# Performance work log

Hardware: AMD Instinct MI355X
Metric: run time of the kernel (lower is better)

## Reference

```python
import jax, jax.numpy as jnp
import numpy as np

B, S, NE, E, H = 4, 2048, 8, 1024, 16
DH = E // H


def setup_inputs() -> dict:
    key = jax.random.key(0)
    ks = jax.random.split(key, 10)
    s = 0.02
    return {
        "x": jax.random.normal(ks[0], (B, S, E), dtype=jnp.float32),
        "w1": jax.random.normal(ks[1], (NE, 4 * E, E), dtype=jnp.float32) * s,
        "b1": jnp.zeros((NE, 4 * E), dtype=jnp.float32),
        "w2": jax.random.normal(ks[2], (NE, E, 4 * E), dtype=jnp.float32) * s,
        "b2": jnp.zeros((NE, E), dtype=jnp.float32),
        "in_proj_w": jax.random.normal(ks[3], (3 * E, E), dtype=jnp.float32) * s,
        "in_proj_b": jnp.zeros((3 * E,), dtype=jnp.float32),
        "out_w": jax.random.normal(ks[4], (E, E), dtype=jnp.float32) * s,
        "out_b": jnp.zeros((E,), dtype=jnp.float32),
        "expert_id": 3,
    }


def reference(x, w1, b1, w2, b2, in_proj_w, in_proj_b, out_w, out_b, expert_id):
    # Per-expert FFN: [B,S,E] -> [B,S,NE,E]
    h = jax.nn.relu(jnp.einsum("bse,nfe->bsnf", x, w1) + b1)
    eo = jnp.einsum("bsnf,nef->bsne", h, w2) + b2  # [B,S,NE,E]

    # Multihead self-attention over the expert axis, batched over (B,S).
    wq, wk, wv = in_proj_w[:E], in_proj_w[E:2 * E], in_proj_w[2 * E:]
    bq, bk, bv = in_proj_b[:E], in_proj_b[E:2 * E], in_proj_b[2 * E:]
    q = (eo @ wq.T + bq).reshape(B, S, NE, H, DH)
    k = (eo @ wk.T + bk).reshape(B, S, NE, H, DH)
    v = (eo @ wv.T + bv).reshape(B, S, NE, H, DH)

    scale = 1.0 / jnp.sqrt(jnp.asarray(DH, dtype=q.dtype))
    # torch additive float mask: tril of ONES added to logits (not -inf masking)
    add_mask = jnp.tril(jnp.ones((NE, NE), dtype=q.dtype))
    logits = jnp.einsum("bsqhd,bskhd->bshqk", q, k) * scale + add_mask
    attn = jax.nn.softmax(logits, axis=-1)
    o = jnp.einsum("bshqk,bskhd->bsqhd", attn, v).reshape(B, S, NE, E)
    o = o @ out_w.T + out_b  # [B,S,NE,E]

    return o[:, :, expert_id, :]  # [B,S,E]
```

## Files before the change

### kernel.cpp

```cpp
#include <hip/hip_runtime.h>

typedef __bf16 bf16x8 __attribute__((ext_vector_type(8)));
typedef float  f32x4  __attribute__((ext_vector_type(4)));

__device__ __forceinline__ float bf2f(unsigned short u) {
    union { unsigned int i; float f; } x; x.i = ((unsigned int)u) << 16; return x.f;
}
__device__ __forceinline__ unsigned short f2bf(float f) {
    union { float f; unsigned int i; } x; x.f = f;
    unsigned int r = x.i + 0x7fff + ((x.i >> 16) & 1);
    return (unsigned short)(r >> 16);
}

__device__ __forceinline__ void gload16(const void* g, void* l) {
    __builtin_amdgcn_global_load_lds(
        (const __attribute__((address_space(1))) void*)g,
        (__attribute__((address_space(3))) void*)l, 16, 0, 0);
}

__global__ __launch_bounds__(256) void cvt_f32_bf16(
    const float4* __restrict__ in, ushort4* __restrict__ out, long n4)
{
    long i = (long)blockIdx.x * blockDim.x + threadIdx.x;
    const long stride = (long)gridDim.x * blockDim.x;
    for (; i < n4; i += stride) {
        const float4 v = in[i];
        ushort4 o = { f2bf(v.x), f2bf(v.y), f2bf(v.z), f2bf(v.w) };
        out[i] = o;
    }
}


template<bool RELU, typename CT>
__global__ __launch_bounds__(256, 4) void gemm_nt(
    const ushort* __restrict__ A, long lda, long sAz,
    const ushort* __restrict__ B, long ldb, long sBz,
    const float* __restrict__ bias, long sBiasz,
    CT* __restrict__ C, long ldc, long sCz,
    int K)
{
    const long z = blockIdx.z;
    A    += z * sAz;
    B    += z * sBz;
    bias += z * sBiasz;
    C    += z * sCz;

    __shared__ alignas(16) ushort As[128 * 32];
    __shared__ alignas(16) ushort Bs[128 * 32];

    const int t    = threadIdx.x;
    const int w    = t >> 6;
    const int lane = t & 63;
    const int lr   = lane & 15;
    const int lq   = lane >> 4;
    const int wm   = (w >> 1) * 64;
    const int wn   = (w & 1) * 64;
    const long m0  = (long)blockIdx.y * 128;
    const long n0  = (long)blockIdx.x * 128;

    const int srow   = t >> 2;
    const int schunk = (t & 3) * 8;
    const ushort* aG = A + (m0 + srow) * lda + schunk;
    const ushort* bG = B + (n0 + srow) * ldb + schunk;
    char* lA = (char*)As + w * 1024;
    char* lB = (char*)Bs + w * 1024;

    f32x4 acc[4][4];
#pragma unroll
    for (int i = 0; i < 4; i++)
#pragma unroll
        for (int j = 0; j < 4; j++) acc[i][j] = (f32x4){0.f, 0.f, 0.f, 0.f};

    for (int kt = 0; kt < K; kt += 32) {
        gload16(aG,            lA);
        gload16(aG + 64 * lda, lA + 4096);
        gload16(bG,            lB);
        gload16(bG + 64 * ldb, lB + 4096);
        aG += 32; bG += 32;
        __syncthreads();

        bf16x8 af[4], bf[4];
#pragma unroll
        for (int i = 0; i < 4; i++)
            af[i] = *(const bf16x8*)&As[(wm + i * 16 + lr) * 32 + lq * 8];
#pragma unroll
        for (int j = 0; j < 4; j++)
            bf[j] = *(const bf16x8*)&Bs[(wn + j * 16 + lr) * 32 + lq * 8];
#pragma unroll
        for (int i = 0; i < 4; i++)
#pragma unroll
            for (int j = 0; j < 4; j++)
                acc[i][j] = __builtin_amdgcn_mfma_f32_16x16x32_bf16(af[i], bf[j], acc[i][j], 0, 0, 0);
        __syncthreads();
    }

#pragma unroll
    for (int j = 0; j < 4; j++) {
        const long col = n0 + wn + j * 16 + lr;
        const float bv = bias[col];
#pragma unroll
        for (int i = 0; i < 4; i++) {
            const long rbase = m0 + wm + i * 16 + lq * 4;
#pragma unroll
            for (int r = 0; r < 4; r++) {
                float v = acc[i][j][r] + bv;
                if (RELU) v = fmaxf(v, 0.f);
                if constexpr (__is_same(CT, ushort)) C[(rbase + r) * ldc + col] = f2bf(v);
                else                                 C[(rbase + r) * ldc + col] = v;
            }
        }
    }
}

__global__ __launch_bounds__(256, 4) void gemm_qkv(
    const ushort* __restrict__ A, long lda, long sAz,
    const ushort* __restrict__ B, long ldb,
    const float* __restrict__ bias,
    ushort* __restrict__ qc,
    ushort* __restrict__ kvc,
    int K, const int* __restrict__ eid_p)
{
    const long z   = blockIdx.z;
    const long n0  = (long)blockIdx.x * 128;
    const bool isq = (n0 < 1024);
    if (isq && z != (long)(*eid_p)) return;
    A += z * sAz;

    __shared__ alignas(16) ushort As[128 * 32];
    __shared__ alignas(16) ushort Bs[128 * 32];

    const int t    = threadIdx.x;
    const int w    = t >> 6;
    const int lane = t & 63;
    const int lr   = lane & 15;
    const int lq   = lane >> 4;
    const int wm   = (w >> 1) * 64;
    const int wn   = (w & 1) * 64;
    const long m0  = (long)blockIdx.y * 128;

    const int srow   = t >> 2;
    const int schunk = (t & 3) * 8;
    const ushort* aG = A + (m0 + srow) * lda + schunk;
    const ushort* bG = B + (n0 + srow) * ldb + schunk;
    char* lA = (char*)As + w * 1024;
    char* lB = (char*)Bs + w * 1024;

    f32x4 acc[4][4];
#pragma unroll
    for (int i = 0; i < 4; i++)
#pragma unroll
        for (int j = 0; j < 4; j++) acc[i][j] = (f32x4){0.f, 0.f, 0.f, 0.f};

    for (int kt = 0; kt < K; kt += 32) {
        gload16(aG,            lA);
        gload16(aG + 64 * lda, lA + 4096);
        gload16(bG,            lB);
        gload16(bG + 64 * ldb, lB + 4096);
        aG += 32; bG += 32;
        __syncthreads();

        bf16x8 af[4], bf[4];
#pragma unroll
        for (int i = 0; i < 4; i++)
            af[i] = *(const bf16x8*)&As[(wm + i * 16 + lr) * 32 + lq * 8];
#pragma unroll
        for (int j = 0; j < 4; j++)
            bf[j] = *(const bf16x8*)&Bs[(wn + j * 16 + lr) * 32 + lq * 8];
#pragma unroll
        for (int i = 0; i < 4; i++)
#pragma unroll
            for (int j = 0; j < 4; j++)
                acc[i][j] = __builtin_amdgcn_mfma_f32_16x16x32_bf16(af[i], bf[j], acc[i][j], 0, 0, 0);
        __syncthreads();
    }

#pragma unroll
    for (int j = 0; j < 4; j++) {
        const long col = n0 + wn + j * 16 + lr;
        const float bv = bias[col];
#pragma unroll
        for (int i = 0; i < 4; i++) {
            const long rbase = m0 + wm + i * 16 + lq * 4;
#pragma unroll
            for (int r = 0; r < 4; r++) {
                const float v = acc[i][j][r] + bv;
                const long row = rbase + r;
                if (isq) qc[row * 1024 + col] = f2bf(v);
                else     kvc[row * 16384 + z * 2048 + (col - 1024)] = f2bf(v);
            }
        }
    }
}

__global__ __launch_bounds__(256) void attn_kernel(
    const ushort* __restrict__ qc, const ushort* __restrict__ kvc,
    const int* __restrict__ eid_p, ushort* __restrict__ o3)
{
    const size_t m = blockIdx.x;
    const int t    = threadIdx.x;
    const int h    = t >> 4;
    const int d0   = (t & 15) * 4;
    const int eid  = *eid_p;

    const ushort4 qu = *(const ushort4*)(qc + m * 1024 + h * 64 + d0);
    const float qv[4] = { bf2f(qu.x), bf2f(qu.y), bf2f(qu.z), bf2f(qu.w) };

    float l[8];
#pragma unroll
    for (int n = 0; n < 8; n++) {
        const ushort4 ku = *(const ushort4*)(kvc + (m * 8 + n) * 2048 + h * 64 + d0);
        float p = qv[0] * bf2f(ku.x) + qv[1] * bf2f(ku.y) + qv[2] * bf2f(ku.z) + qv[3] * bf2f(ku.w);
        p += __shfl_xor(p, 1);
        p += __shfl_xor(p, 2);
        p += __shfl_xor(p, 4);
        p += __shfl_xor(p, 8);
        l[n] = p * 0.125f + ((n <= eid) ? 1.0f : 0.0f);
    }
    float mx = l[0];
#pragma unroll
    for (int n = 1; n < 8; n++) mx = fmaxf(mx, l[n]);
    float e[8], s = 0.f;
#pragma unroll
    for (int n = 0; n < 8; n++) { e[n] = __expf(l[n] - mx); s += e[n]; }
    const float inv = 1.f / s;

    float o[4] = {0.f, 0.f, 0.f, 0.f};
#pragma unroll
    for (int n = 0; n < 8; n++) {
        const ushort4 vu = *(const ushort4*)(kvc + (m * 8 + n) * 2048 + 1024 + h * 64 + d0);
        const float a = e[n] * inv;
        o[0] += a * bf2f(vu.x); o[1] += a * bf2f(vu.y);
        o[2] += a * bf2f(vu.z); o[3] += a * bf2f(vu.w);
    }
    ushort4 ou = { f2bf(o[0]), f2bf(o[1]), f2bf(o[2]), f2bf(o[3]) };
    *(ushort4*)(o3 + m * 1024 + h * 64 + d0) = ou;
}

extern "C" void kernel_launch(void* const* d_in, const int* in_sizes, int n_in,
                              void* d_out, int out_size, void* d_ws, size_t ws_size,
                              hipStream_t stream)
{
    const float* x   = (const float*)d_in[0];
    const float* w1  = (const float*)d_in[1];
    const float* b1  = (const float*)d_in[2];
    const float* w2  = (const float*)d_in[3];
    const float* b2  = (const float*)d_in[4];
    const float* ipw = (const float*)d_in[5];
    const float* ipb = (const float*)d_in[6];
    const float* ow  = (const float*)d_in[7];
    const float* ob  = (const float*)d_in[8];
    const int*   eid = (const int*)d_in[9];

    char* ws = (char*)d_ws;
    size_t off = 0;
    auto alloc = [&](size_t bytes) { char* p = ws + off; off += (bytes + 255) & ~(size_t)255; return p; };
    ushort* w1b  = (ushort*)alloc(8LL * 4096 * 1024 * 2);
    ushort* w2b  = (ushort*)alloc(8LL * 1024 * 4096 * 2);
    ushort* ipwb = (ushort*)alloc(3LL * 1024 * 1024 * 2);
    ushort* owb  = (ushort*)alloc(1LL * 1024 * 1024 * 2);
    ushort* xb   = (ushort*)alloc(8192LL * 1024 * 2);
    ushort* o3b  = (ushort*)alloc(8192LL * 1024 * 2);
    const size_t fixed = off;

    long Mc = 2048;
    while (Mc > 256 && fixed + (size_t)Mc * 116736 + 2048 > ws_size) Mc >>= 1;
    ushort* hb  = (ushort*)alloc((size_t)Mc * 8 * 4096 * 2);
    ushort* eob = (ushort*)alloc((size_t)Mc * 8 * 1024 * 2);
    ushort* kvc = (ushort*)alloc((size_t)Mc * 8 * 2048 * 2);
    ushort* qc  = (ushort*)alloc((size_t)Mc * 1024 * 2);

    const dim3 blk(256);
    const dim3 cgrid(2048);

    cvt_f32_bf16<<<cgrid, blk, 0, stream>>>((const float4*)w1,  (ushort4*)w1b,  8LL * 4096 * 1024 / 4);
    cvt_f32_bf16<<<cgrid, blk, 0, stream>>>((const float4*)w2,  (ushort4*)w2b,  8LL * 1024 * 4096 / 4);
    cvt_f32_bf16<<<cgrid, blk, 0, stream>>>((const float4*)ipw, (ushort4*)ipwb, 3LL * 1024 * 1024 / 4);
    cvt_f32_bf16<<<cgrid, blk, 0, stream>>>((const float4*)ow,  (ushort4*)owb,  1LL * 1024 * 1024 / 4);
    cvt_f32_bf16<<<cgrid, blk, 0, stream>>>((const float4*)x,   (ushort4*)xb,   8192LL * 1024 / 4);

    for (long m0 = 0; m0 < 8192; m0 += Mc) {
        const unsigned my = (unsigned)(Mc / 128);
        gemm_nt<true, ushort><<<dim3(32, my, 8), blk, 0, stream>>>(
            xb + m0 * 1024, 1024, 0,
            w1b, 1024, 4096LL * 1024,
            b1, 4096,
            hb, 4096, (long)Mc * 4096,
            1024);
        gemm_nt<false, ushort><<<dim3(8, my, 8), blk, 0, stream>>>(
            hb, 4096, (long)Mc * 4096,
            w2b, 4096, 1024LL * 4096,
            b2, 1024,
            eob, 1024, (long)Mc * 1024,
            4096);
        gemm_qkv<<<dim3(24, my, 8), blk, 0, stream>>>(
            eob, 1024, (long)Mc * 1024,
            ipwb, 1024,
            ipb,
            qc, kvc,
            1024, eid);
        attn_kernel<<<dim3((unsigned)Mc), blk, 0, stream>>>(
            qc, kvc, eid, o3b + m0 * 1024);
    }

    gemm_nt<false, float><<<dim3(8, 64, 1), blk, 0, stream>>>(
        o3b, 1024, 0,
        owb, 1024, 0,
        ob, 0,
        (float*)d_out, 1024, 0,
        1024);
}
```

Measured before the change: 2.406 ms.

## Replace 128x128 GEMMs with 256x256 4-stage pipelined swizzled-LDS GEMM kernel

Merges the generic GEMM and the QKV GEMM into one templated 256x256-tile kernel with 512 threads. It keeps a 4-deep ring of LDS buffers filled by async global-to-LDS loads, waiting on vmcnt counts instead of two full barriers per k-step. It also adds an XOR swizzle on the LDS layout to avoid bank conflicts, a workgroup-index remap across XCDs, and raised MFMA issue priority. The larger tiles raise arithmetic intensity but cut the number of workgroups and use more LDS and registers, which may lower occupancy.

```diff
diff --git a/kernel.cpp b/kernel.cpp
--- a/kernel.cpp
+++ b/kernel.cpp
@@ -30,163 +30,123 @@
     }
 }
 
-
-template<bool RELU, typename CT>
-__global__ __launch_bounds__(256, 4) void gemm_nt(
+template<bool RELU, typename CT, bool QKV>
+__global__ __launch_bounds__(512, 2) void gemm256(
     const ushort* __restrict__ A, long lda, long sAz,
     const ushort* __restrict__ B, long ldb, long sBz,
     const float* __restrict__ bias, long sBiasz,
     CT* __restrict__ C, long ldc, long sCz,
-    int K)
-{
-    const long z = blockIdx.z;
+    ushort* __restrict__ qc, ushort* __restrict__ kvc,
+    int K, const int* __restrict__ eid_p)
+{
+    const long z  = blockIdx.z;
+    const int gx  = gridDim.x;
+    const int nwg = gx * gridDim.y;
+    int wg = blockIdx.y * gx + blockIdx.x;
+    if ((nwg & 7) == 0) wg = (wg & 7) * (nwg >> 3) + (wg >> 3);
+    const long n0 = (long)(wg % gx) * 256;
+    const long m0 = (long)(wg / gx) * 256;
+
+    if constexpr (QKV) {
+        if (n0 < 1024 && z != (long)(*eid_p)) return;
+    }
     A    += z * sAz;
     B    += z * sBz;
     bias += z * sBiasz;
-    C    += z * sCz;
-
-    __shared__ alignas(16) ushort As[128 * 32];
-    __shared__ alignas(16) ushort Bs[128 * 32];
+    if constexpr (!QKV) C += z * sCz;
+
+    __shared__ alignas(16) ushort As[4][256 * 32];
+    __shared__ alignas(16) ushort Bs[4][256 * 32];
 
     const int t    = threadIdx.x;
-    const int w    = t >> 6;
+    const int wid  = t >> 6;
     const int lane = t & 63;
     const int lr   = lane & 15;
     const int lq   = lane >> 4;
-    const int wm   = (w >> 1) * 64;
-    const int wn   = (w & 1) * 64;
-    const long m0  = (long)blockIdx.y * 128;
-    const long n0  = (long)blockIdx.x * 128;
-
-    const int srow   = t >> 2;
-    const int schunk = (t & 3) * 8;
-    const ushort* aG = A + (m0 + srow) * lda + schunk;
-    const ushort* bG = B + (n0 + srow) * ldb + schunk;
-    char* lA = (char*)As + w * 1024;
-    char* lB = (char*)Bs + w * 1024;
-
-    f32x4 acc[4][4];
-#pragma unroll
-    for (int i = 0; i < 4; i++)
+    const int wr   = wid >> 2;
+    const int wc   = wid & 3;
+
+    const int d0 = wid * 1024 + lane * 16;
+    const int s0 = d0 ^ (((d0 >> 7) & 3) << 4);
+    const int r0 = s0 >> 6;
+    const int c0 = (s0 & 63) >> 1;
+    const ushort* aG0 = A + (m0 + r0) * lda + c0;
+    const ushort* aG1 = A + (m0 + r0 + 128) * lda + c0;
+    const ushort* bG0 = B + (n0 + r0) * ldb + c0;
+    const ushort* bG1 = B + (n0 + r0 + 128) * ldb + c0;
+    const int ldsOff = wid * 512;
+
+    const int chnk  = lq ^ ((lr >> 1) & 3);
+    const int aBase = (wr * 128 + lr) * 32 + chnk * 8;
+    const int bBase = (wc * 64  + lr) * 32 + chnk * 8;
+
+    const int nt = K >> 5;
+
+    #define STAGE(buf_, kt_) { \
+        const long ko_ = (long)(kt_) * 32; \
+        gload16(aG0 + ko_, (void*)&As[buf_][ldsOff]); \
+        gload16(aG1 + ko_, (void*)&As[buf_][4096 + ldsOff]); \
+        gload16(bG0 + ko_, (void*)&Bs[buf_][ldsOff]); \
+        gload16(bG1 + ko_, (void*)&Bs[buf_][4096 + ldsOff]); }
+
+    STAGE(0, 0)
+    if (nt > 1) STAGE(1, 1)
+    if (nt > 2) STAGE(2, 2)
+
+    f32x4 acc[8][4];
+#pragma unroll
+    for (int i = 0; i < 8; i++)
 #pragma unroll
         for (int j = 0; j < 4; j++) acc[i][j] = (f32x4){0.f, 0.f, 0.f, 0.f};
 
-    for (int kt = 0; kt < K; kt += 32) {
-        gload16(aG,            lA);
-        gload16(aG + 64 * lda, lA + 4096);
-        gload16(bG,            lB);
-        gload16(bG + 64 * ldb, lB + 4096);
-        aG += 32; bG += 32;
-        __syncthreads();
-
-        bf16x8 af[4], bf[4];
-#pragma unroll
-        for (int i = 0; i < 4; i++)
-            af[i] = *(const bf16x8*)&As[(wm + i * 16 + lr) * 32 + lq * 8];
-#pragma unroll
-        for (int j = 0; j < 4; j++)
-            bf[j] = *(const bf16x8*)&Bs[(wn + j * 16 + lr) * 32 + lq * 8];
-#pragma unroll
-        for (int i = 0; i < 4; i++)
+    for (int kt = 0; kt < nt; ++kt) {
+        const int rem = nt - 1 - kt;
+        if (rem >= 2)      asm volatile("s_waitcnt vmcnt(8)" ::: "memory");
+        else if (rem == 1) asm volatile("s_waitcnt vmcnt(4)" ::: "memory");
+        else               asm volatile("s_waitcnt vmcnt(0)" ::: "memory");
+        __builtin_amdgcn_s_barrier();
+        __builtin_amdgcn_sched_barrier(0);
+
+        if (kt + 3 < nt) STAGE((kt + 3) & 3, kt + 3)
+
+        const ushort* as_ = As[kt & 3];
+        const ushort* bs_ = Bs[kt & 3];
+        bf16x8 af[8], bfr[4];
+#pragma unroll
+        for (int i = 0; i < 8; i++) af[i]  = *(const bf16x8*)&as_[aBase + i * 512];
+#pragma unroll
+        for (int j = 0; j < 4; j++) bfr[j] = *(const bf16x8*)&bs_[bBase + j * 512];
+
+        __builtin_amdgcn_s_setprio(1);
+#pragma unroll
+        for (int i = 0; i < 8; i++)
 #pragma unroll
             for (int j = 0; j < 4; j++)
-                acc[i][j] = __builtin_amdgcn_mfma_f32_16x16x32_bf16(af[i], bf[j], acc[i][j], 0, 0, 0);
-        __syncthreads();
-    }
+                acc[i][j] = __builtin_amdgcn_mfma_f32_16x16x32_bf16(af[i], bfr[j], acc[i][j], 0, 0, 0);
+        __builtin_amdgcn_s_setprio(0);
+    }
+    #undef STAGE
 
 #pragma unroll
     for (int j = 0; j < 4; j++) {
-        const long col = n0 + wn + j * 16 + lr;
+        const long col = n0 + wc * 64 + j * 16 + lr;
         const float bv = bias[col];
 #pragma unroll
-        for (int i = 0; i < 4; i++) {
-            const long rbase = m0 + wm + i * 16 + lq * 4;
+        for (int i = 0; i < 8; i++) {
+            const long rbase = m0 + wr * 128 + i * 16 + lq * 4;
 #pragma unroll
             for (int r = 0; r < 4; r++) {
                 float v = acc[i][j][r] + bv;
                 if (RELU) v = fmaxf(v, 0.f);
-                if constexpr (__is_same(CT, ushort)) C[(rbase + r) * ldc + col] = f2bf(v);
-                else                                 C[(rbase + r) * ldc + col] = v;
-            }
-        }
-    }
-}
-
-__global__ __launch_bounds__(256, 4) void gemm_qkv(
-    const ushort* __restrict__ A, long lda, long sAz,
-    const ushort* __restrict__ B, long ldb,
-    const float* __restrict__ bias,
-    ushort* __restrict__ qc,
-    ushort* __restrict__ kvc,
-    int K, const int* __restrict__ eid_p)
-{
-    const long z   = blockIdx.z;
-    const long n0  = (long)blockIdx.x * 128;
-    const bool isq = (n0 < 1024);
-    if (isq && z != (long)(*eid_p)) return;
-    A += z * sAz;
-
-    __shared__ alignas(16) ushort As[128 * 32];
-    __shared__ alignas(16) ushort Bs[128 * 32];
-
-    const int t    = threadIdx.x;
-    const int w    = t >> 6;
-    const int lane = t & 63;
-    const int lr   = lane & 15;
-    const int lq   = lane >> 4;
-    const int wm   = (w >> 1) * 64;
-    const int wn   = (w & 1) * 64;
-    const long m0  = (long)blockIdx.y * 128;
-
-    const int srow   = t >> 2;
-    const int schunk = (t & 3) * 8;
-    const ushort* aG = A + (m0 + srow) * lda + schunk;
-    const ushort* bG = B + (n0 + srow) * ldb + schunk;
-    char* lA = (char*)As + w * 1024;
-    char* lB = (char*)Bs + w * 1024;
-
-    f32x4 acc[4][4];
-#pragma unroll
-    for (int i = 0; i < 4; i++)
-#pragma unroll
-        for (int j = 0; j < 4; j++) acc[i][j] = (f32x4){0.f, 0.f, 0.f, 0.f};
-
-    for (int kt = 0; kt < K; kt += 32) {
-        gload16(aG,            lA);
-        gload16(aG + 64 * lda, lA + 4096);
-        gload16(bG,            lB);
-        gload16(bG + 64 * ldb, lB + 4096);
-        aG += 32; bG += 32;
-        __syncthreads();
-
-        bf16x8 af[4], bf[4];
-#pragma unroll
-        for (int i = 0; i < 4; i++)
-            af[i] = *(const bf16x8*)&As[(wm + i * 16 + lr) * 32 + lq * 8];
-#pragma unroll
-        for (int j = 0; j < 4; j++)
-            bf[j] = *(const bf16x8*)&Bs[(wn + j * 16 + lr) * 32 + lq * 8];
-#pragma unroll
-        for (int i = 0; i < 4; i++)
-#pragma unroll
-            for (int j = 0; j < 4; j++)
-                acc[i][j] = __builtin_amdgcn_mfma_f32_16x16x32_bf16(af[i], bf[j], acc[i][j], 0, 0, 0);
-        __syncthreads();
-    }
-
-#pragma unroll
-    for (int j = 0; j < 4; j++) {
-        const long col = n0 + wn + j * 16 + lr;
-        const float bv = bias[col];
-#pragma unroll
-        for (int i = 0; i < 4; i++) {
-            const long rbase = m0 + wm + i * 16 + lq * 4;
-#pragma unroll
-            for (int r = 0; r < 4; r++) {
-                const float v = acc[i][j][r] + bv;
                 const long row = rbase + r;
-                if (isq) qc[row * 1024 + col] = f2bf(v);
-                else     kvc[row * 16384 + z * 2048 + (col - 1024)] = f2bf(v);
+                if constexpr (QKV) {
+                    if (col < 1024) qc[row * 1024 + col] = f2bf(v);
+                    else            kvc[row * 16384 + z * 2048 + (col - 1024)] = f2bf(v);
+                } else if constexpr (__is_same(CT, ushort)) {
+                    C[row * ldc + col] = f2bf(v);
+                } else {
+                    C[row * ldc + col] = v;
+                }
             }
         }
     }
@@ -270,6 +230,7 @@
     ushort* qc  = (ushort*)alloc((size_t)Mc * 1024 * 2);
 
     const dim3 blk(256);
+    const dim3 blk5(512);
     const dim3 cgrid(2048);
 
     cvt_f32_bf16<<<cgrid, blk, 0, stream>>>((const float4*)w1,  (ushort4*)w1b,  8LL * 4096 * 1024 / 4);
@@ -279,33 +240,33 @@
     cvt_f32_bf16<<<cgrid, blk, 0, stream>>>((const float4*)x,   (ushort4*)xb,   8192LL * 1024 / 4);
 
     for (long m0 = 0; m0 < 8192; m0 += Mc) {
-        const unsigned my = (unsigned)(Mc / 128);
-        gemm_nt<true, ushort><<<dim3(32, my, 8), blk, 0, stream>>>(
+        const unsigned my = (unsigned)(Mc / 256);
+        gemm256<true, ushort, false><<<dim3(16, my, 8), blk5, 0, stream>>>(
             xb + m0 * 1024, 1024, 0,
             w1b, 1024, 4096LL * 1024,
             b1, 4096,
             hb, 4096, (long)Mc * 4096,
-            1024);
-        gemm_nt<false, ushort><<<dim3(8, my, 8), blk, 0, stream>>>(
+            nullptr, nullptr, 1024, eid);
+        gemm256<false, ushort, false><<<dim3(4, my, 8), blk5, 0, stream>>>(
             hb, 4096, (long)Mc * 4096,
             w2b, 4096, 1024LL * 4096,
             b2, 1024,
             eob, 1024, (long)Mc * 1024,
-            4096);
-        gemm_qkv<<<dim3(24, my, 8), blk, 0, stream>>>(
+            nullptr, nullptr, 4096, eid);
+        gemm256<false, ushort, true><<<dim3(12, my, 8), blk5, 0, stream>>>(
             eob, 1024, (long)Mc * 1024,
-            ipwb, 1024,
-            ipb,
-            qc, kvc,
-            1024, eid);
+            ipwb, 1024, 0,
+            ipb, 0,
+            (ushort*)nullptr, 0, 0,
+            qc, kvc, 1024, eid);
         attn_kernel<<<dim3((unsigned)Mc), blk, 0, stream>>>(
             qc, kvc, eid, o3b + m0 * 1024);
     }
 
-    gemm_nt<false, float><<<dim3(8, 64, 1), blk, 0, stream>>>(
+    gemm256<false, float, false><<<dim3(4, 32, 1), blk5, 0, stream>>>(
         o3b, 1024, 0,
         owb, 1024, 0,
         ob, 0,
         (float*)d_out, 1024, 0,
-        1024);
-}
+        nullptr, nullptr, 1024, eid);
+}
```

New measurement: 2.641 ms. 9.7% more time.
